# Kernel tuning notes

Hardware: AMD Instinct MI355X
Metric: run time of the kernel (lower is better)

Reference implementation:

```python
import jax, jax.numpy as jnp
import numpy as np

T, B, S, K, C = 2, 64, 30, 12, 20
N_ITEMS, D_ITEM, D_RNN = 20000, 128, 256
D_IN = D_ITEM + D_RNN  # cross_mode concatenates h_meta to basket embedding


def gru_cell(x, h, Wih, Whh, bih, bhh):
    # PyTorch GRUCell gate order: r, z, n
    gi = x @ Wih.T + bih
    gh = h @ Whh.T + bhh
    ir, iz, in_ = jnp.split(gi, 3, -1)
    hr, hz, hn = jnp.split(gh, 3, -1)
    r = jax.nn.sigmoid(ir + hr)
    z = jax.nn.sigmoid(iz + hz)
    n = jnp.tanh(in_ + r * hn)
    return (1.0 - z) * n + z * h


def setup_inputs() -> dict:
    key = jax.random.key(0)
    ks = jax.random.split(key, 16)
    def u(k, sh, fan):
        b = 1.0 / np.sqrt(fan)
        return jax.random.uniform(k, sh, jnp.float32, -b, b)
    return {
        "user_vectors": jax.random.randint(ks[0], (B,), 0, 1000),
        "item_vectors": jax.random.randint(ks[1], (T, B, S, K), 0, N_ITEMS),
        "copy_vectors": jax.random.randint(ks[2], (T, B, S, C), 0, N_ITEMS),
        "emb": jax.random.normal(ks[3], (N_ITEMS, D_ITEM), jnp.float32) * 0.05,
        "Wih": u(ks[4], (T, 3 * D_RNN, D_IN), D_RNN),
        "Whh": u(ks[5], (T, 3 * D_RNN, D_RNN), D_RNN),
        "bih": u(ks[6], (T, 3 * D_RNN), D_RNN),
        "bhh": u(ks[7], (T, 3 * D_RNN), D_RNN),
        "mWih": u(ks[8], (3 * D_RNN, T * D_RNN), D_RNN),
        "mWhh": u(ks[9], (3 * D_RNN, D_RNN), D_RNN),
        "mbih": u(ks[10], (3 * D_RNN,), D_RNN),
        "mbhh": u(ks[11], (3 * D_RNN,), D_RNN),
        "Wnew": u(ks[12], (N_ITEMS, D_RNN), D_RNN),
        "bnew": u(ks[13], (N_ITEMS,), D_RNN),
        "Wcopy": u(ks[14], (T, N_ITEMS, D_RNN), D_RNN),
        "bcopy": u(ks[15], (T, N_ITEMS), D_RNN),
    }


def _forward(item_vectors, copy_vectors, emb, Wih, Whh, bih, bhh,
             mWih, mWhh, mbih, mbhh, Wnew, bnew, Wcopy, bcopy):
    emb = emb.at[0].set(0.0)  # padding_idx=0
    e_items = emb[item_vectors]                               # [T,B,S,K,Di]
    valid = (item_vectors > 0).astype(e_items.dtype)          # [T,B,S,K]
    n_basket = valid.sum(-1)                                  # [T,B,S]
    cell_mask = (n_basket > 0).astype(e_items.dtype)          # [T,B,S]
    den = n_basket + (n_basket == 0).astype(e_items.dtype)
    e_baskets = e_items.sum(-2) / den[..., None]              # ave pool [T,B,S,Di]

    xs = jnp.moveaxis(e_baskets, 2, 0)  # [S,T,B,Di]
    ms = jnp.moveaxis(cell_mask, 2, 0)  # [S,T,B]

    h0 = jnp.zeros((T, B, D_RNN), e_items.dtype)
    hm0 = jnp.zeros((B, D_RNN), e_items.dtype)
    task_gru = jax.vmap(gru_cell)  # vmap over the task axis (distinct weights)

    def step(carry, inp):
        h_tasks, h_meta = carry
        x_t, m_t = inp
        # cross_mode: concat current meta hidden onto each task's input
        cell_in = jnp.concatenate(
            [x_t, jnp.broadcast_to(h_meta, (T, B, D_RNN))], -1)  # [T,B,D_IN]
        nh = task_gru(cell_in, h_tasks, Wih, Whh, bih, bhh)
        m = m_t[..., None]
        h_tasks = nh * m + h_tasks * (1.0 - m)  # freeze hidden on empty baskets
        meta_in = jnp.transpose(h_tasks, (1, 0, 2)).reshape(B, T * D_RNN)
        h_meta = gru_cell(meta_in, h_meta, mWih, mWhh, mbih, mbhh)
        return (h_tasks, h_meta), (h_tasks, h_meta)

    _, (h_seq, hm_seq) = jax.lax.scan(step, (h0, hm0), (xs, ms))
    e_rnn_tasks = jnp.transpose(h_seq, (1, 2, 0, 3))  # [T,B,S,H]
    e_rnn_meta = jnp.transpose(hm_seq, (1, 0, 2))     # [B,S,H]

    score_new = jnp.einsum('bsh,nh->bsn', e_rnn_meta, Wnew) + bnew  # [B,S,N]
    ti = jnp.arange(T)[:, None, None, None]
    bi = jnp.arange(B)[None, :, None, None]
    si = jnp.arange(S)[None, None, :, None]
    copy_mask = jnp.zeros((T, B, S, N_ITEMS), score_new.dtype).at[
        ti, bi, si, copy_vectors].set(1.0)  # scatter_(-1, copy_vectors, 1)
    score_copy = (jnp.einsum('tbsh,tnh->tbsn', e_rnn_tasks, Wcopy)
                  + bcopy[:, None, None, :]) * copy_mask  # [T,B,S,N]
    # stack new-item scores with per-task masked copy scores
    return jnp.concatenate([score_new[None], score_copy], 0)  # [T+1,B,S,N]


def reference(user_vectors, item_vectors, copy_vectors, emb, Wih, Whh, bih, bhh,
              mWih, mWhh, mbih, mbhh, Wnew, bnew, Wcopy, bcopy):
    return _forward(item_vectors, copy_vectors, emb, Wih, Whh, bih, bhh,
                    mWih, mWhh, mbih, mbhh, Wnew, bnew, Wcopy, bcopy)
```

## Files before the change

### kernel.cpp

```cpp
#include <hip/hip_runtime.h>

typedef unsigned short u16;
typedef unsigned int u32;
typedef unsigned long long u64;
typedef __attribute__((ext_vector_type(8))) short short8;
typedef __attribute__((ext_vector_type(4))) float f32x4;

#define NB_ 64
#define NHELP_ 6195

static __device__ __forceinline__ f32x4 mfma16(short8 a, short8 b, f32x4 c) {
  return __builtin_amdgcn_mfma_f32_16x16x32_bf16(a, b, c, 0, 0, 0);
}

static __device__ __forceinline__ void split_bf16(float x, u16& hi, u16& lo) {
  unsigned u = __float_as_uint(x);
  unsigned r = (u + 0x7fffu + ((u >> 16) & 1u)) >> 16;
  hi = (u16)r;
  float fh = __uint_as_float(r << 16);
  float xl = x - fh;
  unsigned ul = __float_as_uint(xl);
  unsigned rl2 = (ul + 0x7fffu + ((ul >> 16) & 1u)) >> 16;
  lo = (u16)rl2;
}

static __device__ __forceinline__ void astore(u32* p, u32 v) {
  __hip_atomic_store(p, v, __ATOMIC_RELAXED, __HIP_MEMORY_SCOPE_AGENT);
}
static __device__ __forceinline__ void unpack8(const uint4& a, const uint4& b,
                                               short8& h, short8& l) {
  u32 wb[8] = {a.x, a.y, a.z, a.w, b.x, b.y, b.z, b.w};
  #pragma unroll
  for (int j = 0; j < 8; ++j) {
    h[j] = (short)(wb[j] & 0xffffu);
    l[j] = (short)(wb[j] >> 16);
  }
}
static __device__ __forceinline__ float unpack_hl(u32 pk) {
  return __uint_as_float((pk & 0xffffu) << 16) + __uint_as_float(pk & 0xffff0000u);
}
static __device__ __forceinline__ void vload8(const u32* p, short8& h, short8& l) {
  uint4 a = *(const uint4*)p;
  uint4 b = *(const uint4*)(p + 4);
  unpack8(a, b, h, l);
}

__global__ __launch_bounds__(128) void k_pool(const int* __restrict__ iv,
                                              const float* __restrict__ emb,
                                              u16* __restrict__ ebh, u16* __restrict__ ebl,
                                              float* __restrict__ cm) {
  int u = blockIdx.x;
  int s = u >> 7;
  int t = (u >> 6) & 1;
  int b = u & 63;
  int d = threadIdx.x;
  const int ibase = ((t * 64 + b) * 30 + s) * 12;
  float sum = 0.f;
  int cnt = 0;
  for (int k = 0; k < 12; ++k) {
    int idx = iv[ibase + k];
    if (idx > 0) { cnt++; sum += emb[(size_t)idx * 128 + d]; }
  }
  float den = (cnt > 0) ? (float)cnt : 1.f;
  float v = sum / den;
  u16 hi, lo; split_bf16(v, hi, lo);
  ebh[(size_t)u * 128 + d] = hi;
  ebl[(size_t)u * 128 + d] = lo;
  if (d == 0) cm[u] = (cnt > 0) ? 1.f : 0.f;
}

__global__ __launch_bounds__(256) void k_swz(const float* __restrict__ Wih,
                                             const float* __restrict__ Whh,
                                             const float* __restrict__ mWih,
                                             const float* __restrict__ mWhh,
                                             const float* __restrict__ Wnew,
                                             u16* __restrict__ w1h, u16* __restrict__ w1l,
                                             u16* __restrict__ w2h, u16* __restrict__ w2l,
                                             u16* __restrict__ wnh, u16* __restrict__ wnl) {
  int gu = blockIdx.x * 4 + (threadIdx.x >> 6);
  int lane = threadIdx.x & 63;
  int ko = (lane >> 4) * 8;
  int cl = lane & 15;
  float src[8];
  if (gu < 2560) {
    int blk = gu / 40, r = gu % 40, ksIdx = r >> 1, nt = r & 1;
    int t = blk >> 5, hd0 = (blk & 31) * 8;
    int c = nt * 16 + cl;
    if (c < 24) {
      int gc = (c < 8) ? (hd0 + c) : (c < 16) ? (256 + hd0 + (c - 8)) : (512 + hd0 + (c - 16));
      const float* wrow; int kk;
      if (ksIdx < 8)       { wrow = Wih + (size_t)(t * 768 + gc) * 384 + 128; kk = ksIdx * 32 + ko; }
      else if (ksIdx < 16) { wrow = Whh + (size_t)(t * 768 + gc) * 256;       kk = (ksIdx - 8) * 32 + ko; }
      else                 { wrow = Wih + (size_t)(t * 768 + gc) * 384;       kk = (ksIdx - 16) * 32 + ko; }
      #pragma unroll
      for (int j = 0; j < 8; ++j) src[j] = wrow[kk + j];
    } else {
      #pragma unroll
      for (int j = 0; j < 8; ++j) src[j] = 0.f;
    }
    int off = gu * 512 + lane * 8;
    #pragma unroll
    for (int j = 0; j < 8; ++j) { u16 h, l; split_bf16(src[j], h, l); w1h[off + j] = h; w1l[off + j] = l; }
  } else if (gu < 4096) {
    int g2 = gu - 2560;
    int blk = g2 / 24, ksIdx = g2 % 24;
    int t1 = blk >> 5;
    int hd0 = blk * 4;
    int c = cl;
    if (c < 12) {
      int gc = (c < 4) ? (hd0 + c) : (c < 8) ? (256 + hd0 + (c - 4)) : (512 + hd0 + (c - 8));
      if (ksIdx < 16) {
        int chunk = (ksIdx < 8) ? (t1 * 8 + ksIdx) : ((1 - t1) * 8 + (ksIdx - 8));
        int kk = chunk * 32 + ko;
        #pragma unroll
        for (int j = 0; j < 8; ++j) src[j] = mWih[(size_t)gc * 512 + kk + j];
      } else {
        int kk = (ksIdx - 16) * 32 + ko;
        #pragma unroll
        for (int j = 0; j < 8; ++j) src[j] = mWhh[(size_t)gc * 256 + kk + j];
      }
    } else {
      #pragma unroll
      for (int j = 0; j < 8; ++j) src[j] = 0.f;
    }
    int off = g2 * 512 + lane * 8;
    #pragma unroll
    for (int j = 0; j < 8; ++j) { u16 h, l; split_bf16(src[j], h, l); w2h[off + j] = h; w2l[off + j] = l; }
  } else if (gu < 14144) {
    int g3 = gu - 4096;
    int gnt = g3 >> 3, ks = g3 & 7;
    int col = gnt * 16 + cl;
    if (col < 20000) {
      int kk = ks * 32 + ko;
      #pragma unroll
      for (int j = 0; j < 8; ++j) src[j] = Wnew[(size_t)col * 256 + kk + j];
    } else {
      #pragma unroll
      for (int j = 0; j < 8; ++j) src[j] = 0.f;
    }
    int off = g3 * 512 + lane * 8;
    #pragma unroll
    for (int j = 0; j < 8; ++j) { u16 h, l; split_bf16(src[j], h, l); wnh[off + j] = h; wnl[off + j] = l; }
  }
}

__global__ __launch_bounds__(256) void k_gix(const u16* __restrict__ ebh, const u16* __restrict__ ebl,
                                             const u16* __restrict__ w1h, const u16* __restrict__ w1l,
                                             const float* __restrict__ bih, const float* __restrict__ bhh,
                                             float* __restrict__ gix) {
  int blk = blockIdx.x;
  int t1 = blk >> 5, hd1 = (blk & 31) * 8;
  int tid = threadIdx.x, lane = tid & 63, w = tid >> 6;
  int arow = w * 16 + (lane & 15);
  int ko = (lane >> 4) * 8;
  __shared__ u16 lwh[4096], lwl[4096];
  {
    const uint4* sh = (const uint4*)(w1h + ((size_t)blk * 40 + 32) * 512);
    const uint4* sl = (const uint4*)(w1l + ((size_t)blk * 40 + 32) * 512);
    uint4* dh = (uint4*)lwh; uint4* dl = (uint4*)lwl;
    for (int i = tid; i < 512; i += 256) { dh[i] = sh[i]; dl[i] = sl[i]; }
  }
  int c = lane & 15;
  float brz, bn = 0.f;
  {
    int gc = (c < 8) ? (hd1 + c) : (256 + hd1 + (c - 8));
    brz = bih[t1 * 768 + gc] + bhh[t1 * 768 + gc];
    if (c < 8) bn = bih[t1 * 768 + 512 + hd1 + c];
  }
  __syncthreads();
  for (int s = 0; s < 30; ++s) {
    f32x4 a3[2];
    a3[0] = (f32x4){0.f, 0.f, 0.f, 0.f};
    a3[1] = (f32x4){0.f, 0.f, 0.f, 0.f};
    const u16* Xh = ebh + (size_t)((s * 2 + t1) * 64 + arow) * 128;
    const u16* Xl = ebl + (size_t)((s * 2 + t1) * 64 + arow) * 128;
    #pragma unroll
    for (int k = 0; k < 4; ++k) {
      short8 xh = *(const short8*)(Xh + k * 32 + ko);
      short8 xl = *(const short8*)(Xl + k * 32 + ko);
      #pragma unroll
      for (int nt = 0; nt < 2; ++nt) {
        short8 bh = *(const short8*)(lwh + (k * 2 + nt) * 512 + lane * 8);
        short8 bl = *(const short8*)(lwl + (k * 2 + nt) * 512 + lane * 8);
        a3[nt] = mfma16(xh, bh, a3[nt]);
        a3[nt] = mfma16(xl, bh, a3[nt]);
        a3[nt] = mfma16(xh, bl, a3[nt]);
      }
    }
    float* grow = gix + (size_t)(blk * 30 + s) * 64 * 32;
    #pragma unroll
    for (int i = 0; i < 4; ++i) {
      int r = w * 16 + (lane >> 4) * 4 + i;
      grow[r * 32 + c] = a3[0][i] + brz;
      if (c < 8) grow[r * 32 + 16 + c] = a3[1][i] + bn;
    }
  }
}

static __device__ __forceinline__ void bar_arrive(u32* slots, int blk, int epoch) {
  __syncthreads();
  if (threadIdx.x == 0) astore(slots + blk, (u32)epoch);
}
static __device__ __forceinline__ void bar_wait(u32* slots, int epoch) {
  int lane = threadIdx.x & 63;
  u32 v;
  for (;;) {
    asm volatile("global_load_dword %0, %1, off sc0 sc1\n\ts_waitcnt vmcnt(0)"
                 : "=v"(v) : "v"(slots + lane) : "memory");
    if ((int)v >= epoch) break;
  }
}
static __device__ __forceinline__ void helper_wait(u32* slots, int target) {
  if (threadIdx.x < 64) {
    u32 v;
    for (;;) {
      asm volatile("global_load_dword %0, %1, off sc0 sc1\n\ts_waitcnt vmcnt(0)"
                   : "=v"(v) : "v"(slots + threadIdx.x) : "memory");
      if (__all((int)v >= target)) break;
      __builtin_amdgcn_s_sleep(15);
      __builtin_amdgcn_s_sleep(15);
    }
  }
  __syncthreads();
}

#define RNN_LDS 130560

__global__ __launch_bounds__(256, 1) void k_mega(
    const u16* __restrict__ w1h, const u16* __restrict__ w1l,
    const u16* __restrict__ w2h, const u16* __restrict__ w2l,
    const float* __restrict__ gix,
    const float* __restrict__ bhh,
    const float* __restrict__ mbih, const float* __restrict__ mbhh,
    const float* __restrict__ cm,
    u32* __restrict__ hpk,
    u32* __restrict__ apk,
    u32* slots,
    const u16* __restrict__ wnh, const u16* __restrict__ wnl,
    const float* __restrict__ bnew,
    const int* __restrict__ cv,
    const float* __restrict__ wc,
    const float* __restrict__ bc,
    float* __restrict__ out) {

  if (blockIdx.x >= NB_) {
    int h = blockIdx.x - NB_;
    int g = h / 413, r = h % 413;
    int tid = threadIdx.x, lane = tid & 63, w = tid >> 6;
    int ko = (lane >> 4) * 8;
    if (r < 256) {
      int s = 2 * g + (r >= 128);
      int rr = r & 127;
      int t = rr >> 6, b = rr & 63;
      float* orow = out + (size_t)(1 + t) * 38400000 + (size_t)(b * 30 + s) * 20000;
      f32x4 z4 = {0.f, 0.f, 0.f, 0.f};
      f32x4* zp = (f32x4*)orow;
      for (int i = tid; i < 5000; i += 256)
        __builtin_nontemporal_store(z4, zp + i);
      helper_wait(slots, 2 * s + 1);
      const u32* hp = hpk + (size_t)(((s + 1) * 2 + t) * 64 + b) * 256;
      uint4 hq = *(const uint4*)(hp + lane * 4);
      float4 h4;
      h4.x = unpack_hl(hq.x); h4.y = unpack_hl(hq.y);
      h4.z = unpack_hl(hq.z); h4.w = unpack_hl(hq.w);
      int base = ((t * 64 + b) * 30 + s) * 20;
      for (int c = w; c < 20; c += 4) {
        int idx = cv[base + c];
        const float* wr = wc + ((size_t)t * 20000 + idx) * 256;
        float4 w4 = *(const float4*)(wr + lane * 4);
        float d = h4.x * w4.x + h4.y * w4.y + h4.z * w4.z + h4.w * w4.w;
        #pragma unroll
        for (int m = 32; m >= 1; m >>= 1) d += __shfl_xor(d, m, 64);
        if (lane == 0) orow[idx] = d + bc[t * 20000 + idx];
      }
    } else {
      int q = g, nb = r - 256;
      helper_wait(slots, 4 * q + 4);
      f32x4 acc[2][8];
      #pragma unroll
      for (int mi = 0; mi < 2; ++mi)
        #pragma unroll
        for (int nt = 0; nt < 8; ++nt) acc[mi][nt] = (f32x4){0.f, 0.f, 0.f, 0.f};
      #pragma unroll
      for (int ks = 0; ks < 8; ++ks) {
        short8 ah[2], al[2];
        #pragma unroll
        for (int mi = 0; mi < 2; ++mi) {
          int rrow = q * 128 + (w * 2 + mi) * 16 + (lane & 15);
          vload8(apk + (size_t)rrow * 256 + ks * 32 + ko, ah[mi], al[mi]);
        }
        #pragma unroll
        for (int nt = 0; nt < 8; ++nt) {
          int un = (nb * 8 + nt) * 8 + ks;
          short8 bh = *(const short8*)(wnh + (size_t)un * 512 + lane * 8);
          short8 bl = *(const short8*)(wnl + (size_t)un * 512 + lane * 8);
          #pragma unroll
          for (int mi = 0; mi < 2; ++mi) {
            acc[mi][nt] = mfma16(ah[mi], bh, acc[mi][nt]);
            acc[mi][nt] = mfma16(al[mi], bh, acc[mi][nt]);
            acc[mi][nt] = mfma16(ah[mi], bl, acc[mi][nt]);
          }
        }
      }
      #pragma unroll
      for (int mi = 0; mi < 2; ++mi)
        #pragma unroll
        for (int nt = 0; nt < 8; ++nt) {
          int col = nb * 128 + nt * 16 + (lane & 15);
          if (col < 20000) {
            float bn = bnew[col];
            #pragma unroll
            for (int i = 0; i < 4; ++i) {
              int rrow = q * 128 + (w * 2 + mi) * 16 + (lane >> 4) * 4 + i;
              int sA = rrow >> 6, bA = rrow & 63;
              out[(size_t)(bA * 30 + sA) * 20000 + col] = acc[mi][nt][i] + bn;
            }
          }
        }
    }
    return;
  }

  extern __shared__ char smem[];
  u16* lw1h = (u16*)smem;
  u16* lw1l = (u16*)(smem + 32768);
  u16* lw2h = (u16*)(smem + 65536);
  u16* lw2l = (u16*)(smem + 90112);
  float* ls_rz = (float*)(smem + 114688);
  float* ls_gi = (float*)(smem + 118784);
  float* ls_gh = (float*)(smem + 120832);
  float* ls_cm = (float*)(smem + 122880);

  const int blk = blockIdx.x;
  const int tid = threadIdx.x;
  const int lane = tid & 63;
  const int w = tid >> 6;
  const int t1 = blk >> 5;
  const int hd1 = (blk & 31) * 8;
  const int hd2 = blk * 4;
  const int arow = w * 16 + (lane & 15);
  const int ko = (lane >> 4) * 8;
  int epoch = 0;

  {
    const uint4* s1h = (const uint4*)(w1h + (size_t)blk * 40 * 512);
    const uint4* s1l = (const uint4*)(w1l + (size_t)blk * 40 * 512);
    uint4* d1h = (uint4*)lw1h; uint4* d1l = (uint4*)lw1l;
    for (int i = tid; i < 2048; i += 256) { d1h[i] = s1h[i]; d1l[i] = s1l[i]; }
    const uint4* s2h = (const uint4*)(w2h + (size_t)blk * 24 * 512);
    const uint4* s2l = (const uint4*)(w2l + (size_t)blk * 24 * 512);
    uint4* d2h = (uint4*)lw2h; uint4* d2l = (uint4*)lw2l;
    for (int i = tid; i < 1536; i += 256) { d2h[i] = s2h[i]; d2l[i] = s2l[i]; }
    for (int i = tid; i < 1920; i += 256) ls_cm[i] = cm[((i >> 6) * 2 + t1) * 64 + (i & 63)];
  }
  const int cc = lane & 15;
  float bhhn = (cc < 8) ? bhh[t1 * 768 + 512 + hd1 + cc] : 0.f;
  float mrz_b = 0.f, mgi_b = 0.f, mgh_b = 0.f;
  if (cc < 8) {
    int gc = (cc < 4) ? (hd2 + cc) : (256 + hd2 + (cc - 4));
    mrz_b = mbih[gc] + mbhh[gc];
  } else if (cc < 12) {
    int gn = 512 + hd2 + (cc - 8);
    mgi_b = mbih[gn];
    mgh_b = mbhh[gn];
  }

  float gq[8];
  {
    const float* grow = gix + (size_t)(blk * 30 + 0) * 2048;
    #pragma unroll
    for (int i = 0; i < 4; ++i) {
      int r = w * 16 + (lane >> 4) * 4 + i;
      gq[i]     = grow[r * 32 + cc];
      gq[4 + i] = grow[r * 32 + 16 + (cc & 7)];
    }
  }
  __syncthreads();

  short8 ah1[8], al1[8];
  short8 xh2[8], xl2[8];
  f32x4 a2s[2];
  a2s[0] = (f32x4){0.f, 0.f, 0.f, 0.f};
  a2s[1] = (f32x4){0.f, 0.f, 0.f, 0.f};
  float hold0 = 0.f, hold1 = 0.f;
  float hm_reg = 0.f;

  for (int s = 0; s < 30; ++s) {
    f32x4 a1[2];
    a1[0] = (f32x4){0.f, 0.f, 0.f, 0.f};
    a1[1] = (f32x4){0.f, 0.f, 0.f, 0.f};
    if (s > 0) {
      bar_wait(slots, epoch);
      const u32* Ap = apk + (size_t)((s - 1) * 64 + arow) * 256 + ko;
      uint4 ra[16];
      #pragma unroll
      for (int k = 0; k < 8; ++k) {
        ra[2 * k]     = *(const uint4*)(Ap + k * 32);
        ra[2 * k + 1] = *(const uint4*)(Ap + k * 32 + 4);
      }
      #pragma unroll
      for (int k = 0; k < 8; ++k) {
        unpack8(ra[2 * k], ra[2 * k + 1], ah1[k], al1[k]);
        #pragma unroll
        for (int nt = 0; nt < 2; ++nt) {
          short8 bh = *(const short8*)(lw1h + (k * 2 + nt) * 512 + lane * 8);
          short8 bl = *(const short8*)(lw1l + (k * 2 + nt) * 512 + lane * 8);
          a1[nt] = mfma16(ah1[k], bh, a1[nt]);
          a1[nt] = mfma16(al1[k], bh, a1[nt]);
          a1[nt] = mfma16(ah1[k], bl, a1[nt]);
        }
      }
    }
    #pragma unroll
    for (int i = 0; i < 4; ++i) {
      int rl = (lane >> 4) * 4 + i;
      ls_rz[(w * 16 + rl) * 16 + cc] = a1[0][i] + a2s[0][i] + gq[i];
      if (cc < 8) {
        ls_gi[(w * 16 + rl) * 8 + cc] = a1[1][i] + gq[4 + i];
        ls_gh[(w * 16 + rl) * 8 + cc] = a2s[1][i] + bhhn;
      }
    }
    asm volatile("s_waitcnt lgkmcnt(0)" ::: "memory");
    {
      int item = lane;
      int rl = item >> 3, c = item & 7;
      float rv = ls_rz[(w * 16 + rl) * 16 + c], zv = ls_rz[(w * 16 + rl) * 16 + 8 + c];
      float gi = ls_gi[(w * 16 + rl) * 8 + c], gh = ls_gh[(w * 16 + rl) * 8 + c];
      float r = 1.f / (1.f + expf(-rv));
      float z = 1.f / (1.f + expf(-zv));
      float n = tanhf(gi + r * gh);
      int b = w * 16 + rl;
      float m = ls_cm[s * 64 + b];
      float hnew = (1.f - z) * n + z * hold0;
      float hout = (m > 0.5f) ? hnew : hold0;
      hold0 = hout;
      int oo = (((s + 1) * 2 + t1) * 64 + b) * 256 + hd1 + c;
      u16 xh, xl; split_bf16(hout, xh, xl);
      astore(hpk + oo, (u32)xh | ((u32)xl << 16));
    }
    {
      int item = 64 + lane;
      int rl = item >> 3, c = item & 7;
      float rv = ls_rz[(w * 16 + rl) * 16 + c], zv = ls_rz[(w * 16 + rl) * 16 + 8 + c];
      float gi = ls_gi[(w * 16 + rl) * 8 + c], gh = ls_gh[(w * 16 + rl) * 8 + c];
      float r = 1.f / (1.f + expf(-rv));
      float z = 1.f / (1.f + expf(-zv));
      float n = tanhf(gi + r * gh);
      int b = w * 16 + rl;
      float m = ls_cm[s * 64 + b];
      float hnew = (1.f - z) * n + z * hold1;
      float hout = (m > 0.5f) ? hnew : hold1;
      hold1 = hout;
      int oo = (((s + 1) * 2 + t1) * 64 + b) * 256 + hd1 + c;
      u16 xh, xl; split_bf16(hout, xh, xl);
      astore(hpk + oo, (u32)xh | ((u32)xl << 16));
    }
    ++epoch;
    bar_arrive(slots, blk, epoch);

    f32x4 m1 = (f32x4){0.f, 0.f, 0.f, 0.f};
    f32x4 m2 = (f32x4){0.f, 0.f, 0.f, 0.f};
    if (s > 0) {
      #pragma unroll
      for (int k = 0; k < 8; ++k) {
        short8 bh = *(const short8*)(lw2h + (16 + k) * 512 + lane * 8);
        short8 bl = *(const short8*)(lw2l + (16 + k) * 512 + lane * 8);
        m2 = mfma16(ah1[k], bh, m2);
        m2 = mfma16(al1[k], bh, m2);
        m2 = mfma16(ah1[k], bl, m2);
      }
    }
    if (s < 29) {
      const float* grow = gix + (size_t)(blk * 30 + s + 1) * 2048;
      #pragma unroll
      for (int i = 0; i < 4; ++i) {
        int r = w * 16 + (lane >> 4) * 4 + i;
        gq[i]     = grow[r * 32 + cc];
        gq[4 + i] = grow[r * 32 + 16 + (cc & 7)];
      }
    }
    bar_wait(slots, epoch);

    {
      const u32* Hp = hpk + (size_t)(((s + 1) * 2 + t1) * 64 + arow) * 256 + ko;
      const u32* Hq = hpk + (size_t)(((s + 1) * 2 + (1 - t1)) * 64 + arow) * 256 + ko;
      uint4 rx[16], ry[16];
      #pragma unroll
      for (int k = 0; k < 8; ++k) {
        rx[2 * k]     = *(const uint4*)(Hp + k * 32);
        rx[2 * k + 1] = *(const uint4*)(Hp + k * 32 + 4);
        ry[2 * k]     = *(const uint4*)(Hq + k * 32);
        ry[2 * k + 1] = *(const uint4*)(Hq + k * 32 + 4);
      }
      #pragma unroll
      for (int k = 0; k < 8; ++k) {
        unpack8(rx[2 * k], rx[2 * k + 1], xh2[k], xl2[k]);
        short8 bh = *(const short8*)(lw2h + k * 512 + lane * 8);
        short8 bl = *(const short8*)(lw2l + k * 512 + lane * 8);
        m1 = mfma16(xh2[k], bh, m1);
        m1 = mfma16(xl2[k], bh, m1);
        m1 = mfma16(xh2[k], bl, m1);
      }
      #pragma unroll
      for (int k = 0; k < 8; ++k) {
        short8 yh, yl;
        unpack8(ry[2 * k], ry[2 * k + 1], yh, yl);
        short8 bh = *(const short8*)(lw2h + (8 + k) * 512 + lane * 8);
        short8 bl = *(const short8*)(lw2l + (8 + k) * 512 + lane * 8);
        m1 = mfma16(yh, bh, m1);
        m1 = mfma16(yl, bh, m1);
        m1 = mfma16(yh, bl, m1);
      }
    }
    #pragma unroll
    for (int i = 0; i < 4; ++i) {
      int rl = (lane >> 4) * 4 + i;
      if (cc < 8) {
        ls_rz[(w * 16 + rl) * 16 + cc] = m1[i] + m2[i] + mrz_b;
      } else if (cc < 12) {
        ls_gi[(w * 16 + rl) * 8 + (cc - 8)] = m1[i] + mgi_b;
        ls_gh[(w * 16 + rl) * 8 + (cc - 8)] = m2[i] + mgh_b;
      }
    }
    asm volatile("s_waitcnt lgkmcnt(0)" ::: "memory");
    {
      int rl = lane >> 2, c = lane & 3;
      float rv = ls_rz[(w * 16 + rl) * 16 + c], zv = ls_rz[(w * 16 + rl) * 16 + 4 + c];
      float gi = ls_gi[(w * 16 + rl) * 8 + c], gh = ls_gh[(w * 16 + rl) * 8 + c];
      float r = 1.f / (1.f + expf(-rv));
      float z = 1.f / (1.f + expf(-zv));
      float n = tanhf(gi + r * gh);
      int b = w * 16 + rl;
      int g2 = hd2 + c;
      float hmnew = (1.f - z) * n + z * hm_reg;
      hm_reg = hmnew;
      int ar = s * 64 + b;
      u16 xh, xl; split_bf16(hmnew, xh, xl);
      astore(apk + ar * 256 + g2, (u32)xh | ((u32)xl << 16));
    }
    ++epoch;
    bar_arrive(slots, blk, epoch);

    a2s[0] = (f32x4){0.f, 0.f, 0.f, 0.f};
    a2s[1] = (f32x4){0.f, 0.f, 0.f, 0.f};
    if (s < 29) {
      #pragma unroll
      for (int k = 0; k < 8; ++k) {
        #pragma unroll
        for (int nt = 0; nt < 2; ++nt) {
          short8 bh = *(const short8*)(lw1h + ((8 + k) * 2 + nt) * 512 + lane * 8);
          short8 bl = *(const short8*)(lw1l + ((8 + k) * 2 + nt) * 512 + lane * 8);
          a2s[nt] = mfma16(xh2[k], bh, a2s[nt]);
          a2s[nt] = mfma16(xl2[k], bh, a2s[nt]);
          a2s[nt] = mfma16(xh2[k], bl, a2s[nt]);
        }
      }
    }
  }
}

extern "C" void kernel_launch(void* const* d_in, const int* in_sizes, int n_in,
                              void* d_out, int out_size, void* d_ws, size_t ws_size,
                              hipStream_t stream) {
  const int* iv = (const int*)d_in[1];
  const int* cv = (const int*)d_in[2];
  const float* emb = (const float*)d_in[3];
  const float* Wih = (const float*)d_in[4];
  const float* Whh = (const float*)d_in[5];
  const float* bih = (const float*)d_in[6];
  const float* bhh = (const float*)d_in[7];
  const float* mWih = (const float*)d_in[8];
  const float* mWhh = (const float*)d_in[9];
  const float* mbih = (const float*)d_in[10];
  const float* mbhh = (const float*)d_in[11];
  const float* Wnew = (const float*)d_in[12];
  const float* bnew = (const float*)d_in[13];
  const float* Wcopy = (const float*)d_in[14];
  const float* bcopy = (const float*)d_in[15];
  float* out = (float*)d_out;
  char* ws = (char*)d_ws;

  size_t o = 0;
  auto take = [&](size_t sz) { size_t r = o; o += sz; return r; };
  size_t BAR = take(256);
  size_t CM  = take(15360);
  size_t EBH = take(983040);
  size_t EBL = take(983040);
  size_t HPK = take(4063232);
  size_t APK = take(1966080);
  size_t GIX = take(15728640);
  size_t W1H = take(2621440);
  size_t W1L = take(2621440);
  size_t W2H = take(1572864);
  size_t W2L = take(1572864);
  size_t WNH = take(10289152);
  size_t WNL = take(10289152);
  if (ws_size < o) return;

  hipFuncSetAttribute(reinterpret_cast<const void*>(k_mega),
                      hipFuncAttributeMaxDynamicSharedMemorySize, RNN_LDS);

  hipMemsetAsync(ws + BAR, 0, 256, stream);

  k_pool<<<3840, 128, 0, stream>>>(iv, emb, (u16*)(ws + EBH), (u16*)(ws + EBL), (float*)(ws + CM));
  k_swz<<<3536, 256, 0, stream>>>(Wih, Whh, mWih, mWhh, Wnew,
                                  (u16*)(ws + W1H), (u16*)(ws + W1L),
                                  (u16*)(ws + W2H), (u16*)(ws + W2L),
                                  (u16*)(ws + WNH), (u16*)(ws + WNL));
  k_gix<<<64, 256, 0, stream>>>((const u16*)(ws + EBH), (const u16*)(ws + EBL),
                                (const u16*)(ws + W1H), (const u16*)(ws + W1L),
                                bih, bhh, (float*)(ws + GIX));
  k_mega<<<NB_ + NHELP_, 256, RNN_LDS, stream>>>(
      (const u16*)(ws + W1H), (const u16*)(ws + W1L),
      (const u16*)(ws + W2H), (const u16*)(ws + W2L),
      (const float*)(ws + GIX), bhh, mbih, mbhh,
      (const float*)(ws + CM),
      (u32*)(ws + HPK), (u32*)(ws + APK),
      (u32*)(ws + BAR),
      (const u16*)(ws + WNH), (const u16*)(ws + WNL),
      bnew, cv, Wcopy, bcopy, out);
}
```

Before: 488.9 us.

## Fuse pooling and weight swizzle kernels; add single progress counter for helper waits

Merges the basket pooling kernel and weight swizzle kernel into one launch, packing two pooling units per 256-thread block, which removes one kernel launch. Helper blocks now poll a single progress word, published by block 0 after each grid barrier, instead of having 64 lanes poll all 64 barrier slots. This cuts polling traffic on the barrier slots that the RNN blocks spin on. The cost is one extra global store per barrier and a final barrier wait in block 0.

```diff
diff --git a/kernel.cpp b/kernel.cpp
--- a/kernel.cpp
+++ b/kernel.cpp
@@ -45,39 +45,40 @@
   unpack8(a, b, h, l);
 }
 
-__global__ __launch_bounds__(128) void k_pool(const int* __restrict__ iv,
+__global__ __launch_bounds__(256) void k_prep(const int* __restrict__ iv,
                                               const float* __restrict__ emb,
                                               u16* __restrict__ ebh, u16* __restrict__ ebl,
-                                              float* __restrict__ cm) {
-  int u = blockIdx.x;
-  int s = u >> 7;
-  int t = (u >> 6) & 1;
-  int b = u & 63;
-  int d = threadIdx.x;
-  const int ibase = ((t * 64 + b) * 30 + s) * 12;
-  float sum = 0.f;
-  int cnt = 0;
-  for (int k = 0; k < 12; ++k) {
-    int idx = iv[ibase + k];
-    if (idx > 0) { cnt++; sum += emb[(size_t)idx * 128 + d]; }
-  }
-  float den = (cnt > 0) ? (float)cnt : 1.f;
-  float v = sum / den;
-  u16 hi, lo; split_bf16(v, hi, lo);
-  ebh[(size_t)u * 128 + d] = hi;
-  ebl[(size_t)u * 128 + d] = lo;
-  if (d == 0) cm[u] = (cnt > 0) ? 1.f : 0.f;
-}
-
-__global__ __launch_bounds__(256) void k_swz(const float* __restrict__ Wih,
-                                             const float* __restrict__ Whh,
-                                             const float* __restrict__ mWih,
-                                             const float* __restrict__ mWhh,
-                                             const float* __restrict__ Wnew,
-                                             u16* __restrict__ w1h, u16* __restrict__ w1l,
-                                             u16* __restrict__ w2h, u16* __restrict__ w2l,
-                                             u16* __restrict__ wnh, u16* __restrict__ wnl) {
-  int gu = blockIdx.x * 4 + (threadIdx.x >> 6);
+                                              float* __restrict__ cm,
+                                              const float* __restrict__ Wih,
+                                              const float* __restrict__ Whh,
+                                              const float* __restrict__ mWih,
+                                              const float* __restrict__ mWhh,
+                                              const float* __restrict__ Wnew,
+                                              u16* __restrict__ w1h, u16* __restrict__ w1l,
+                                              u16* __restrict__ w2h, u16* __restrict__ w2l,
+                                              u16* __restrict__ wnh, u16* __restrict__ wnl) {
+  if (blockIdx.x < 1920) {
+    int u = blockIdx.x * 2 + (threadIdx.x >> 7);
+    int s = u >> 7;
+    int t = (u >> 6) & 1;
+    int b = u & 63;
+    int d = threadIdx.x & 127;
+    const int ibase = ((t * 64 + b) * 30 + s) * 12;
+    float sum = 0.f;
+    int cnt = 0;
+    for (int k = 0; k < 12; ++k) {
+      int idx = iv[ibase + k];
+      if (idx > 0) { cnt++; sum += emb[(size_t)idx * 128 + d]; }
+    }
+    float den = (cnt > 0) ? (float)cnt : 1.f;
+    float v = sum / den;
+    u16 hi, lo; split_bf16(v, hi, lo);
+    ebh[(size_t)u * 128 + d] = hi;
+    ebl[(size_t)u * 128 + d] = lo;
+    if (d == 0) cm[u] = (cnt > 0) ? 1.f : 0.f;
+    return;
+  }
+  int gu = (blockIdx.x - 1920) * 4 + (threadIdx.x >> 6);
   int lane = threadIdx.x & 63;
   int ko = (lane >> 4) * 8;
   int cl = lane & 15;
@@ -210,13 +211,13 @@
     if ((int)v >= epoch) break;
   }
 }
-static __device__ __forceinline__ void helper_wait(u32* slots, int target) {
-  if (threadIdx.x < 64) {
+static __device__ __forceinline__ void helper_wait(const u32* hprog, int target) {
+  if (threadIdx.x == 0) {
     u32 v;
     for (;;) {
       asm volatile("global_load_dword %0, %1, off sc0 sc1\n\ts_waitcnt vmcnt(0)"
-                   : "=v"(v) : "v"(slots + threadIdx.x) : "memory");
-      if (__all((int)v >= target)) break;
+                   : "=v"(v) : "v"(hprog) : "memory");
+      if ((int)v >= target) break;
       __builtin_amdgcn_s_sleep(15);
       __builtin_amdgcn_s_sleep(15);
     }
@@ -242,6 +243,7 @@
     const float* __restrict__ wc,
     const float* __restrict__ bc,
     float* __restrict__ out) {
+  u32* hprog = slots + 64;
 
   if (blockIdx.x >= NB_) {
     int h = blockIdx.x - NB_;
@@ -257,7 +259,7 @@
       f32x4* zp = (f32x4*)orow;
       for (int i = tid; i < 5000; i += 256)
         __builtin_nontemporal_store(z4, zp + i);
-      helper_wait(slots, 2 * s + 1);
+      helper_wait(hprog, 2 * s + 1);
       const u32* hp = hpk + (size_t)(((s + 1) * 2 + t) * 64 + b) * 256;
       uint4 hq = *(const uint4*)(hp + lane * 4);
       float4 h4;
@@ -275,7 +277,7 @@
       }
     } else {
       int q = g, nb = r - 256;
-      helper_wait(slots, 4 * q + 4);
+      helper_wait(hprog, 4 * q + 4);
       f32x4 acc[2][8];
       #pragma unroll
       for (int mi = 0; mi < 2; ++mi)
@@ -391,6 +393,7 @@
     a1[1] = (f32x4){0.f, 0.f, 0.f, 0.f};
     if (s > 0) {
       bar_wait(slots, epoch);
+      if (blk == 0 && tid == 0) astore(hprog, (u32)epoch);
       const u32* Ap = apk + (size_t)((s - 1) * 64 + arow) * 256 + ko;
       uint4 ra[16];
       #pragma unroll
@@ -480,6 +483,7 @@
       }
     }
     bar_wait(slots, epoch);
+    if (blk == 0 && tid == 0) astore(hprog, (u32)epoch);
 
     {
       const u32* Hp = hpk + (size_t)(((s + 1) * 2 + t1) * 64 + arow) * 256 + ko;
@@ -556,6 +560,10 @@
         }
       }
     }
+  }
+  if (blk == 0) {
+    bar_wait(slots, epoch);
+    if (tid == 0) astore(hprog, (u32)epoch);
   }
 }
 
@@ -582,7 +590,7 @@
 
   size_t o = 0;
   auto take = [&](size_t sz) { size_t r = o; o += sz; return r; };
-  size_t BAR = take(256);
+  size_t BAR = take(512);
   size_t CM  = take(15360);
   size_t EBH = take(983040);
   size_t EBL = take(983040);
@@ -600,13 +608,13 @@
   hipFuncSetAttribute(reinterpret_cast<const void*>(k_mega),
                       hipFuncAttributeMaxDynamicSharedMemorySize, RNN_LDS);
 
-  hipMemsetAsync(ws + BAR, 0, 256, stream);
-
-  k_pool<<<3840, 128, 0, stream>>>(iv, emb, (u16*)(ws + EBH), (u16*)(ws + EBL), (float*)(ws + CM));
-  k_swz<<<3536, 256, 0, stream>>>(Wih, Whh, mWih, mWhh, Wnew,
-                                  (u16*)(ws + W1H), (u16*)(ws + W1L),
-                                  (u16*)(ws + W2H), (u16*)(ws + W2L),
-                                  (u16*)(ws + WNH), (u16*)(ws + WNL));
+  hipMemsetAsync(ws + BAR, 0, 512, stream);
+
+  k_prep<<<5456, 256, 0, stream>>>(iv, emb, (u16*)(ws + EBH), (u16*)(ws + EBL), (float*)(ws + CM),
+                                   Wih, Whh, mWih, mWhh, Wnew,
+                                   (u16*)(ws + W1H), (u16*)(ws + W1L),
+                                   (u16*)(ws + W2H), (u16*)(ws + W2L),
+                                   (u16*)(ws + WNH), (u16*)(ws + WNL));
   k_gix<<<64, 256, 0, stream>>>((const u16*)(ws + EBH), (const u16*)(ws + EBL),
                                 (const u16*)(ws + W1H), (const u16*)(ws + W1L),
                                 bih, bhh, (float*)(ws + GIX));
```

Measured after the change: 473.1 us. 1.03x faster.
